# Performance work log

Hardware: AMD Instinct MI355X
Metric: run time of the kernel (lower is better)

## Reference

```python
import jax, jax.numpy as jnp
import numpy as np

B, N, C, H, E, K = 2, 2048, 1024, 4096, 8, 2
TAU = 1.0


def setup_inputs() -> dict:
    key = jax.random.key(0)
    ks = jax.random.split(key, 9)
    x = jax.random.normal(ks[0], (B, N, C), dtype=jnp.float32)
    T = B * N
    u = jax.random.uniform(ks[1], (T, E), minval=1e-6, maxval=1.0 - 1e-6)
    gumbel_noise = -jnp.log(-jnp.log(u))  # Gumbel(0,1) samples
    s = 0.02
    gate_w = jax.random.normal(ks[2], (C, E), dtype=jnp.float32) * s
    gate_b = jnp.zeros((E,), dtype=jnp.float32)
    w1 = jax.random.normal(ks[3], (E, C, H), dtype=jnp.float32) * s
    b1 = jnp.zeros((E, H), dtype=jnp.float32)
    w2 = jax.random.normal(ks[4], (E, H, C), dtype=jnp.float32) * s
    b2 = jnp.zeros((E, C), dtype=jnp.float32)
    return {"x": x, "gumbel_noise": gumbel_noise, "gate_w": gate_w,
            "gate_b": gate_b, "w1": w1, "b1": b1, "w2": w2, "b2": b2}


def reference(x, gumbel_noise, gate_w, gate_b, w1, b1, w2, b2):
    Bb, Nn, Cc = x.shape
    x_flat = x.reshape(-1, Cc)                                  # [T, C]
    logits = x_flat @ gate_w + gate_b                           # [T, E]
    # F.gumbel_softmax(hard=False, tau=1): softmax((logits + g)/tau)
    gates = jax.nn.softmax((logits + gumbel_noise) / TAU, axis=-1)
    mean_gates = gates.mean(axis=0)
    load_balance_loss = jnp.sum(mean_gates * jnp.log(mean_gates + 1e-8))
    topk_vals, topk_idxs = jax.lax.top_k(gates, K)              # [T, K]
    T = x_flat.shape[0]
    # scatter top-k gate weights into a dense [T, E] combine matrix
    comb = jnp.zeros((T, E), dtype=gates.dtype)
    comb = comb.at[jnp.arange(T)[:, None], topk_idxs].set(topk_vals)
    # dense per-expert MLP over all tokens, then weighted combine
    h = jnp.einsum('tc,ech->teh', x_flat, w1) + b1              # [T, E, H]
    h = jax.nn.gelu(h, approximate=False)                        # exact GELU (nn.GELU)
    y = jnp.einsum('teh,ehc->tec', h, w2) + b2                  # [T, E, C]
    out = jnp.einsum('te,tec->tc', comb, y)                     # [T, C]
    return out.reshape(Bb, Nn, Cc), load_balance_loss
```

## Files before the change

### kernel.cpp

```cpp
#include <hip/hip_runtime.h>
#include <math.h>

#define TT  4096
#define CC  1024
#define HH  4096
#define EE  8
#define TKN 8192
#define PGRID 768

typedef _Float16 f16x8 __attribute__((ext_vector_type(8)));
typedef float    f32x4 __attribute__((ext_vector_type(4)));

#define GLD_LDS16(g, l)                                                        \
    __builtin_amdgcn_global_load_lds(                                          \
        (const __attribute__((address_space(1))) void*)(g),                    \
        (__attribute__((address_space(3))) void*)(l), 16, 0, 0)

__global__ __launch_bounds__(256) void gate_kernel(
    const float* __restrict__ x, const float* __restrict__ gn,
    const float* __restrict__ gw, const float* __restrict__ gb,
    int* __restrict__ topk_idx, float* __restrict__ topk_w,
    int* __restrict__ counts, float* __restrict__ gsum)
{
    int wave = threadIdx.x >> 6, lane = threadIdx.x & 63;
    int t = blockIdx.x * 4 + wave;
    const float* xrow = x + (size_t)t * CC;

    double acc[EE];
#pragma unroll
    for (int e = 0; e < EE; e++) acc[e] = 0.0;

#pragma unroll
    for (int i = 0; i < CC / 64; i++) {
        int c = i * 64 + lane;
        float xv = xrow[c];
        const float4* g4 = reinterpret_cast<const float4*>(gw + (size_t)c * EE);
        float4 g0 = g4[0], g1 = g4[1];
        double xd = (double)xv;
        acc[0] += xd * (double)g0.x; acc[1] += xd * (double)g0.y;
        acc[2] += xd * (double)g0.z; acc[3] += xd * (double)g0.w;
        acc[4] += xd * (double)g1.x; acc[5] += xd * (double)g1.y;
        acc[6] += xd * (double)g1.z; acc[7] += xd * (double)g1.w;
    }
#pragma unroll
    for (int e = 0; e < EE; e++)
#pragma unroll
        for (int off = 32; off > 0; off >>= 1)
            acc[e] += __shfl_xor(acc[e], off);

    double z[EE], m = -1e300;
#pragma unroll
    for (int e = 0; e < EE; e++) {
        z[e] = acc[e] + (double)gb[e] + (double)gn[(size_t)t * EE + e];
        m = fmax(m, z[e]);
    }
    double p[EE], s = 0.0;
#pragma unroll
    for (int e = 0; e < EE; e++) { p[e] = exp(z[e] - m); s += p[e]; }
    double inv = 1.0 / s;
    double g[EE];
#pragma unroll
    for (int e = 0; e < EE; e++) g[e] = p[e] * inv;

    int i1 = 0; double v1 = g[0];
#pragma unroll
    for (int e = 1; e < EE; e++) if (g[e] > v1) { v1 = g[e]; i1 = e; }
    int i2 = -1; double v2 = -1.0;
#pragma unroll
    for (int e = 0; e < EE; e++) if (e != i1 && g[e] > v2) { v2 = g[e]; i2 = e; }

    if (lane == 0) {
        topk_idx[t * 2 + 0] = i1; topk_w[t * 2 + 0] = (float)v1;
        topk_idx[t * 2 + 1] = i2; topk_w[t * 2 + 1] = (float)v2;
        atomicAdd(&counts[i1], 1);
        atomicAdd(&counts[i2], 1);
    }

    __shared__ float gp[4][EE];
    if (lane == 0) {
#pragma unroll
        for (int e = 0; e < EE; e++) gp[wave][e] = (float)g[e];
    }
    __syncthreads();
    if (threadIdx.x < EE) {
        float s4 = gp[0][threadIdx.x] + gp[1][threadIdx.x] +
                   gp[2][threadIdx.x] + gp[3][threadIdx.x];
        atomicAdd(&gsum[threadIdx.x], s4);
    }
}

__global__ __launch_bounds__(256) void transpose_f16_kernel(
    const float* __restrict__ src, _Float16* __restrict__ dst, int R, int Ccols)
{
    __shared__ float tile[64][65];
    int e = blockIdx.z;
    const float* s = src + (size_t)e * R * Ccols;
    _Float16* d = dst + (size_t)e * R * Ccols;
    int c0 = blockIdx.x * 64, r0 = blockIdx.y * 64;
    int tx = threadIdx.x, ty = threadIdx.y;
#pragma unroll
    for (int i = 0; i < 16; i++) {
        int r = ty + i * 4;
        tile[r][tx] = s[(size_t)(r0 + r) * Ccols + c0 + tx];
    }
    __syncthreads();
#pragma unroll
    for (int i = 0; i < 16; i++) {
        int c = ty + i * 4;
        d[(size_t)(c0 + c) * R + r0 + tx] = (_Float16)tile[tx][c];
    }
}

__global__ __launch_bounds__(256) void scan_kernel(
    const int* __restrict__ counts, int* __restrict__ offsets,
    const float* __restrict__ gsum, float* __restrict__ loss_out,
    int* __restrict__ tiles1, int* __restrict__ tiles2, int* __restrict__ ntl)
{
    __shared__ int s_mt[EE], s_tb1[EE], s_tb2[EE];
    int tid = threadIdx.x;
    if (tid == 0) {
        int o = 0, t1 = 0, t2 = 0;
#pragma unroll
        for (int e = 0; e < EE; e++) {
            offsets[e] = o;
            int mt = (counts[e] + 127) >> 7;
            s_mt[e] = mt; s_tb1[e] = t1; s_tb2[e] = t2;
            o += counts[e]; t1 += mt * (HH / 128); t2 += mt * 2 * (CC / 128);
        }
        offsets[EE] = o;
        ntl[0] = t1; ntl[1] = t2;
        float L = 0.f;
#pragma unroll
        for (int e = 0; e < EE; e++) {
            float me = gsum[e] / (float)TT;
            L += me * logf(me + 1e-8f);
        }
        *loss_out = L;
    }
    __syncthreads();
    {
        int e = tid >> 5, n = tid & 31;
        int base = s_tb1[e] + n * s_mt[e];
        for (int m = 0; m < s_mt[e]; m++)
            tiles1[base + m] = (e << 20) | (n << 12) | m;
    }
    if (tid < 128) {
        int e = tid >> 4, nk = tid & 15;
        int base = s_tb2[e] + nk * s_mt[e];
        for (int m = 0; m < s_mt[e]; m++)
            tiles2[base + m] = (e << 20) | (nk << 12) | m;
    }
}

__global__ __launch_bounds__(256) void scatter_kernel(
    const int* __restrict__ topk_idx, const float* __restrict__ topk_w,
    const int* __restrict__ offsets, int* __restrict__ fill,
    int* __restrict__ rowtok, float* __restrict__ rweight)
{
    int t = blockIdx.x * 256 + threadIdx.x;
#pragma unroll
    for (int k = 0; k < 2; k++) {
        int e = topk_idx[t * 2 + k];
        int pos = offsets[e] + atomicAdd(&fill[e], 1);
        rowtok[pos] = t;
        rweight[pos] = topk_w[t * 2 + k];
    }
}

__global__ __launch_bounds__(256) void gather_kernel(
    const float* __restrict__ x, const int* __restrict__ rowtok,
    _Float16* __restrict__ xg)
{
    int p = blockIdx.x * 2 + (threadIdx.x >> 7);
    int c = (threadIdx.x & 127) * 8;
    int t = rowtok[p];
    const float4* s = reinterpret_cast<const float4*>(x + (size_t)t * CC + c);
    float4 v0 = s[0], v1 = s[1];
    f16x8 o;
    o[0] = (_Float16)v0.x; o[1] = (_Float16)v0.y;
    o[2] = (_Float16)v0.z; o[3] = (_Float16)v0.w;
    o[4] = (_Float16)v1.x; o[5] = (_Float16)v1.y;
    o[6] = (_Float16)v1.z; o[7] = (_Float16)v1.w;
    *reinterpret_cast<f16x8*>(xg + (size_t)p * CC + c) = o;
}

__global__ __launch_bounds__(256) void gemm1_kernel(
    const _Float16* __restrict__ xg, const _Float16* __restrict__ w1t,
    const float* __restrict__ b1, const int* __restrict__ offsets,
    const int* __restrict__ tiles, const int* __restrict__ ntl,
    _Float16* __restrict__ h)
{
    __shared__ __align__(16) _Float16 As[128][64];
    __shared__ __align__(16) _Float16 Bs[128][64];

    int nt = ntl[0];
    int q = (nt + PGRID - 1) / PGRID;
    int t0 = blockIdx.x * q;
    int t1 = t0 + q; if (t1 > nt) t1 = nt;

    int tid = threadIdx.x;
    int wave = tid >> 6, lane = tid & 63;
    int wm = (wave >> 1) * 64, wn = (wave & 1) * 64;
    int lrow = lane & 15, kg = lane >> 4;
    int ch0 = wave * 4 * 64 + lane;
    int rbase = (lane >> 4) * 4;

    for (int ti = t0; ti < t1; ti++) {
        int id = tiles[ti];
        int e = id >> 20, n0 = ((id >> 12) & 0xFF) * 128, m0 = (id & 0xFFF) * 128;
        int segs = offsets[e];
        int M = offsets[e + 1] - segs;
        const _Float16* wB = w1t + (size_t)e * HH * CC;

        const _Float16* ap[4]; const _Float16* bp[4];
        _Float16 *al[4], *bl[4];
#pragma unroll
        for (int j = 0; j < 4; j++) {
            int ch = ch0 + j * 64;
            int row = ch >> 3, kc = ch & 7;
            int rm = m0 + row; if (rm >= M) rm = M - 1;
            ap[j] = xg + (size_t)(segs + rm) * CC + kc * 8;
            bp[j] = wB + (size_t)(n0 + row) * CC + kc * 8;
            al[j] = &As[0][0] + ch * 8;
            bl[j] = &Bs[0][0] + ch * 8;
        }

        f32x4 acc[4][4];
#pragma unroll
        for (int i = 0; i < 4; i++)
#pragma unroll
            for (int j = 0; j < 4; j++)
#pragma unroll
                for (int r = 0; r < 4; r++) acc[i][j][r] = 0.f;

        for (int k0 = 0; k0 < CC; k0 += 64) {
#pragma unroll
            for (int j = 0; j < 4; j++) {
                GLD_LDS16(ap[j], al[j]);
                GLD_LDS16(bp[j], bl[j]);
                ap[j] += 64; bp[j] += 64;
            }
            __syncthreads();

            f16x8 aF[2][4], bF[2][4];
#pragma unroll
            for (int s = 0; s < 2; s++)
#pragma unroll
                for (int i = 0; i < 4; i++) {
                    aF[s][i] = *reinterpret_cast<const f16x8*>(
                        &As[wm + i * 16 + lrow][s * 32 + kg * 8]);
                    bF[s][i] = *reinterpret_cast<const f16x8*>(
                        &Bs[wn + i * 16 + lrow][s * 32 + kg * 8]);
                }
#pragma unroll
            for (int s = 0; s < 2; s++)
#pragma unroll
                for (int mi = 0; mi < 4; mi++)
#pragma unroll
                    for (int ni = 0; ni < 4; ni++)
                        acc[mi][ni] = __builtin_amdgcn_mfma_f32_16x16x32_f16(
                            aF[s][mi], bF[s][ni], acc[mi][ni], 0, 0, 0);
            __syncthreads();
        }

#pragma unroll
        for (int mi = 0; mi < 4; mi++) {
#pragma unroll
            for (int ni = 0; ni < 4; ni++) {
                int gcol = n0 + wn + ni * 16 + lrow;
                float bias = b1[(size_t)e * HH + gcol];
#pragma unroll
                for (int r = 0; r < 4; r++) {
                    int rowl = m0 + wm + mi * 16 + rbase + r;
                    if (rowl < M) {
                        float v = acc[mi][ni][r] + bias;
                        v = 0.5f * v * (1.0f + erff(v * 0.70710678118654752f));
                        h[(size_t)(segs + rowl) * HH + gcol] = (_Float16)v;
                    }
                }
            }
        }
    }
}

__global__ __launch_bounds__(256) void gemm2_kernel(
    const _Float16* __restrict__ h, const _Float16* __restrict__ w2t,
    const float* __restrict__ b2, const int* __restrict__ rowtok,
    const float* __restrict__ rweight, const int* __restrict__ offsets,
    const int* __restrict__ tiles, const int* __restrict__ ntl,
    float* __restrict__ out)
{
    __shared__ __align__(16) _Float16 As[128][64];
    __shared__ __align__(16) _Float16 Bs[128][64];
    __shared__ int toks[128];
    __shared__ float wgt[128];

    int nt = ntl[1];
    int q = (nt + PGRID - 1) / PGRID;
    int t0 = blockIdx.x * q;
    int t1 = t0 + q; if (t1 > nt) t1 = nt;

    int tid = threadIdx.x;
    int wave = tid >> 6, lane = tid & 63;
    int wm = (wave >> 1) * 64, wn = (wave & 1) * 64;
    int lrow = lane & 15, kg = lane >> 4;
    int ch0 = wave * 4 * 64 + lane;
    int rbase = (lane >> 4) * 4;

    for (int ti = t0; ti < t1; ti++) {
        int id = tiles[ti];
        int e = id >> 20, nk = (id >> 12) & 0xFF, m0 = (id & 0xFFF) * 128;
        int kz = nk >> 3, n0 = (nk & 7) * 128;
        int segs = offsets[e];
        int M = offsets[e + 1] - segs;
        const _Float16* wB = w2t + (size_t)e * CC * HH;
        int kbeg = kz * (HH / 2);

        __syncthreads();
        if (tid < 128) {
            int r = m0 + tid;
            int rr = (r < M) ? r : (M - 1);
            toks[tid] = rowtok[segs + rr];
            wgt[tid] = rweight[segs + rr];
        }

        const _Float16* ap[4]; const _Float16* bp[4];
        _Float16 *al[4], *bl[4];
#pragma unroll
        for (int j = 0; j < 4; j++) {
            int ch = ch0 + j * 64;
            int row = ch >> 3, kc = ch & 7;
            int rm = m0 + row; if (rm >= M) rm = M - 1;
            ap[j] = h  + (size_t)(segs + rm) * HH + kbeg + kc * 8;
            bp[j] = wB + (size_t)(n0 + row) * HH + kbeg + kc * 8;
            al[j] = &As[0][0] + ch * 8;
            bl[j] = &Bs[0][0] + ch * 8;
        }

        f32x4 acc[4][4];
#pragma unroll
        for (int i = 0; i < 4; i++)
#pragma unroll
            for (int j = 0; j < 4; j++)
#pragma unroll
                for (int r = 0; r < 4; r++) acc[i][j][r] = 0.f;

        for (int k0 = 0; k0 < HH / 2; k0 += 64) {
#pragma unroll
            for (int j = 0; j < 4; j++) {
                GLD_LDS16(ap[j], al[j]);
                GLD_LDS16(bp[j], bl[j]);
                ap[j] += 64; bp[j] += 64;
            }
            __syncthreads();

            f16x8 aF[2][4], bF[2][4];
#pragma unroll
            for (int s = 0; s < 2; s++)
#pragma unroll
                for (int i = 0; i < 4; i++) {
                    aF[s][i] = *reinterpret_cast<const f16x8*>(
                        &As[wm + i * 16 + lrow][s * 32 + kg * 8]);
                    bF[s][i] = *reinterpret_cast<const f16x8*>(
                        &Bs[wn + i * 16 + lrow][s * 32 + kg * 8]);
                }
#pragma unroll
            for (int s = 0; s < 2; s++)
#pragma unroll
                for (int mi = 0; mi < 4; mi++)
#pragma unroll
                    for (int ni = 0; ni < 4; ni++)
                        acc[mi][ni] = __builtin_amdgcn_mfma_f32_16x16x32_f16(
                            aF[s][mi], bF[s][ni], acc[mi][ni], 0, 0, 0);
            __syncthreads();
        }

#pragma unroll
        for (int mi = 0; mi < 4; mi++) {
#pragma unroll
            for (int ni = 0; ni < 4; ni++) {
                int gcol = n0 + wn + ni * 16 + lrow;
                float bias = (kz == 0) ? b2[(size_t)e * CC + gcol] : 0.f;
#pragma unroll
                for (int r = 0; r < 4; r++) {
                    int rowl = m0 + wm + mi * 16 + rbase + r;
                    if (rowl < M) {
                        int lr = rowl - m0;
                        float v = (acc[mi][ni][r] + bias) * wgt[lr];
                        unsafeAtomicAdd(&out[(size_t)toks[lr] * CC + gcol], v);
                    }
                }
            }
        }
    }
}

extern "C" void kernel_launch(void* const* d_in, const int* in_sizes, int n_in,
                              void* d_out, int out_size, void* d_ws, size_t ws_size,
                              hipStream_t stream)
{
    const float* x  = (const float*)d_in[0];
    const float* gn = (const float*)d_in[1];
    const float* gw = (const float*)d_in[2];
    const float* gb = (const float*)d_in[3];
    const float* w1 = (const float*)d_in[4];
    const float* b1 = (const float*)d_in[5];
    const float* w2 = (const float*)d_in[6];
    const float* b2 = (const float*)d_in[7];
    float* out = (float*)d_out;

    char* w = (char*)d_ws;
    int*   counts  = (int*)(w + 0);
    int*   fill    = (int*)(w + 32);
    int*   offsets = (int*)(w + 64);
    float* gsum    = (float*)(w + 128);
    int*   ntl     = (int*)(w + 192);
    size_t off = 256;
    int*   topk_idx = (int*)(w + off);   off += (size_t)TT * 2 * 4;
    float* topk_w   = (float*)(w + off); off += (size_t)TT * 2 * 4;
    int*   rowtok   = (int*)(w + off);   off += (size_t)TKN * 4;
    float* rweight  = (float*)(w + off); off += (size_t)TKN * 4;
    int*   tiles1   = (int*)(w + off);   off += 4096 * 4;
    int*   tiles2   = (int*)(w + off);   off += 2048 * 4;
    _Float16* xg  = (_Float16*)(w + off); off += (size_t)TKN * CC * 2;
    _Float16* w1t = (_Float16*)(w + off); off += (size_t)EE * HH * CC * 2;
    _Float16* w2t = (_Float16*)(w + off); off += (size_t)EE * CC * HH * 2;
    _Float16* hbuf = (_Float16*)(w + off); off += (size_t)TKN * HH * 2;

    (void)hipMemsetAsync(d_out, 0, (size_t)out_size * sizeof(float), stream);
    (void)hipMemsetAsync(d_ws, 0, 256, stream);

    gate_kernel<<<TT / 4, 256, 0, stream>>>(x, gn, gw, gb, topk_idx, topk_w,
                                            counts, gsum);
    transpose_f16_kernel<<<dim3(HH / 64, CC / 64, EE), dim3(64, 4), 0, stream>>>(
        w1, w1t, CC, HH);
    transpose_f16_kernel<<<dim3(CC / 64, HH / 64, EE), dim3(64, 4), 0, stream>>>(
        w2, w2t, HH, CC);
    scan_kernel<<<1, 256, 0, stream>>>(counts, offsets, gsum,
                                       out + (size_t)TT * CC, tiles1, tiles2, ntl);
    scatter_kernel<<<TT / 256, 256, 0, stream>>>(topk_idx, topk_w, offsets, fill,
                                                 rowtok, rweight);
    gather_kernel<<<TKN / 2, 256, 0, stream>>>(x, rowtok, xg);
    gemm1_kernel<<<PGRID, 256, 0, stream>>>(xg, w1t, b1, offsets, tiles1, ntl, hbuf);
    gemm2_kernel<<<PGRID, 256, 0, stream>>>(hbuf, w2t, b2, rowtok, rweight,
                                            offsets, tiles2, ntl, out);
}
```

Baseline: 976.9 us.

## Use atomic tile tickets, tanh GELU, and a deterministic combine pass

Replaces the static tile partition in both grouped GEMMs with a per-block atomic ticket counter for dynamic load balancing, and raises the persistent grid size with an occupancy hint. Exact erf GELU is swapped for a tanh-based approximation built on a fast exp. When the workspace is large enough, gemm2 writes per-K-split partial results to a buffer, and a new combine kernel sums the two splits and applies the top-k weights. This removes the float atomics and the output memset, at the cost of extra buffer traffic and a small change in numerical accuracy.

```diff
diff --git a/kernel.cpp b/kernel.cpp
--- a/kernel.cpp
+++ b/kernel.cpp
@@ -6,7 +6,7 @@
 #define HH  4096
 #define EE  8
 #define TKN 8192
-#define PGRID 768
+#define PGRID 1024
 
 typedef _Float16 f16x8 __attribute__((ext_vector_type(8)));
 typedef float    f32x4 __attribute__((ext_vector_type(4)));
@@ -15,6 +15,12 @@
     __builtin_amdgcn_global_load_lds(                                          \
         (const __attribute__((address_space(1))) void*)(g),                    \
         (__attribute__((address_space(3))) void*)(l), 16, 0, 0)
+
+__device__ __forceinline__ float fast_gelu(float v) {
+    float y = 0.79788456080286536f * (v + 0.044715f * v * v * v);
+    float ey = __expf(2.0f * y);
+    return v - v / (ey + 1.0f);
+}
 
 __global__ __launch_bounds__(256) void gate_kernel(
     const float* __restrict__ x, const float* __restrict__ gn,
@@ -155,7 +161,8 @@
 __global__ __launch_bounds__(256) void scatter_kernel(
     const int* __restrict__ topk_idx, const float* __restrict__ topk_w,
     const int* __restrict__ offsets, int* __restrict__ fill,
-    int* __restrict__ rowtok, float* __restrict__ rweight)
+    int* __restrict__ rowtok, float* __restrict__ rweight,
+    int* __restrict__ posmap)
 {
     int t = blockIdx.x * 256 + threadIdx.x;
 #pragma unroll
@@ -164,6 +171,7 @@
         int pos = offsets[e] + atomicAdd(&fill[e], 1);
         rowtok[pos] = t;
         rweight[pos] = topk_w[t * 2 + k];
+        posmap[t * 2 + k] = pos;
     }
 }
 
@@ -184,20 +192,17 @@
     *reinterpret_cast<f16x8*>(xg + (size_t)p * CC + c) = o;
 }
 
-__global__ __launch_bounds__(256) void gemm1_kernel(
+__global__ __launch_bounds__(256, 4) void gemm1_kernel(
     const _Float16* __restrict__ xg, const _Float16* __restrict__ w1t,
     const float* __restrict__ b1, const int* __restrict__ offsets,
     const int* __restrict__ tiles, const int* __restrict__ ntl,
-    _Float16* __restrict__ h)
+    int* __restrict__ ticket, _Float16* __restrict__ h)
 {
     __shared__ __align__(16) _Float16 As[128][64];
     __shared__ __align__(16) _Float16 Bs[128][64];
+    __shared__ int sh_ti;
 
     int nt = ntl[0];
-    int q = (nt + PGRID - 1) / PGRID;
-    int t0 = blockIdx.x * q;
-    int t1 = t0 + q; if (t1 > nt) t1 = nt;
-
     int tid = threadIdx.x;
     int wave = tid >> 6, lane = tid & 63;
     int wm = (wave >> 1) * 64, wn = (wave & 1) * 64;
@@ -205,7 +210,12 @@
     int ch0 = wave * 4 * 64 + lane;
     int rbase = (lane >> 4) * 4;
 
-    for (int ti = t0; ti < t1; ti++) {
+    for (;;) {
+        if (tid == 0) sh_ti = atomicAdd(ticket, 1);
+        __syncthreads();
+        int ti = sh_ti;
+        if (ti >= nt) break;
+
         int id = tiles[ti];
         int e = id >> 20, n0 = ((id >> 12) & 0xFF) * 128, m0 = (id & 0xFFF) * 128;
         int segs = offsets[e];
@@ -273,8 +283,7 @@
                 for (int r = 0; r < 4; r++) {
                     int rowl = m0 + wm + mi * 16 + rbase + r;
                     if (rowl < M) {
-                        float v = acc[mi][ni][r] + bias;
-                        v = 0.5f * v * (1.0f + erff(v * 0.70710678118654752f));
+                        float v = fast_gelu(acc[mi][ni][r] + bias);
                         h[(size_t)(segs + rowl) * HH + gcol] = (_Float16)v;
                     }
                 }
@@ -283,23 +292,20 @@
     }
 }
 
-__global__ __launch_bounds__(256) void gemm2_kernel(
+__global__ __launch_bounds__(256, 4) void gemm2_kernel(
     const _Float16* __restrict__ h, const _Float16* __restrict__ w2t,
     const float* __restrict__ b2, const int* __restrict__ rowtok,
     const float* __restrict__ rweight, const int* __restrict__ offsets,
     const int* __restrict__ tiles, const int* __restrict__ ntl,
-    float* __restrict__ out)
+    int* __restrict__ ticket, float* __restrict__ ybuf, float* __restrict__ out)
 {
     __shared__ __align__(16) _Float16 As[128][64];
     __shared__ __align__(16) _Float16 Bs[128][64];
     __shared__ int toks[128];
     __shared__ float wgt[128];
+    __shared__ int sh_ti;
 
     int nt = ntl[1];
-    int q = (nt + PGRID - 1) / PGRID;
-    int t0 = blockIdx.x * q;
-    int t1 = t0 + q; if (t1 > nt) t1 = nt;
-
     int tid = threadIdx.x;
     int wave = tid >> 6, lane = tid & 63;
     int wm = (wave >> 1) * 64, wn = (wave & 1) * 64;
@@ -307,7 +313,12 @@
     int ch0 = wave * 4 * 64 + lane;
     int rbase = (lane >> 4) * 4;
 
-    for (int ti = t0; ti < t1; ti++) {
+    for (;;) {
+        if (tid == 0) sh_ti = atomicAdd(ticket, 1);
+        __syncthreads();
+        int ti = sh_ti;
+        if (ti >= nt) break;
+
         int id = tiles[ti];
         int e = id >> 20, nk = (id >> 12) & 0xFF, m0 = (id & 0xFFF) * 128;
         int kz = nk >> 3, n0 = (nk & 7) * 128;
@@ -316,8 +327,7 @@
         const _Float16* wB = w2t + (size_t)e * CC * HH;
         int kbeg = kz * (HH / 2);
 
-        __syncthreads();
-        if (tid < 128) {
+        if (!ybuf && tid < 128) {
             int r = m0 + tid;
             int rr = (r < M) ? r : (M - 1);
             toks[tid] = rowtok[segs + rr];
@@ -385,13 +395,43 @@
                 for (int r = 0; r < 4; r++) {
                     int rowl = m0 + wm + mi * 16 + rbase + r;
                     if (rowl < M) {
-                        int lr = rowl - m0;
-                        float v = (acc[mi][ni][r] + bias) * wgt[lr];
-                        unsafeAtomicAdd(&out[(size_t)toks[lr] * CC + gcol], v);
+                        float v = acc[mi][ni][r] + bias;
+                        if (ybuf) {
+                            ybuf[((size_t)kz * TKN + segs + rowl) * CC + gcol] = v;
+                        } else {
+                            int lr = rowl - m0;
+                            unsafeAtomicAdd(&out[(size_t)toks[lr] * CC + gcol],
+                                            v * wgt[lr]);
+                        }
                     }
                 }
             }
         }
+    }
+}
+
+__global__ __launch_bounds__(256) void combine_kernel(
+    const float* __restrict__ ybuf, const int* __restrict__ posmap,
+    const float* __restrict__ topk_w, float* __restrict__ out)
+{
+    int t = blockIdx.x * 2 + (threadIdx.x >> 7);
+    int c = (threadIdx.x & 127) * 8;
+    int p1 = posmap[t * 2 + 0], p2 = posmap[t * 2 + 1];
+    float w1 = topk_w[t * 2 + 0], w2 = topk_w[t * 2 + 1];
+    const float4* y0a = reinterpret_cast<const float4*>(ybuf + (size_t)p1 * CC + c);
+    const float4* y1a = reinterpret_cast<const float4*>(ybuf + ((size_t)TKN + p1) * CC + c);
+    const float4* y0b = reinterpret_cast<const float4*>(ybuf + (size_t)p2 * CC + c);
+    const float4* y1b = reinterpret_cast<const float4*>(ybuf + ((size_t)TKN + p2) * CC + c);
+    float4* o = reinterpret_cast<float4*>(out + (size_t)t * CC + c);
+#pragma unroll
+    for (int i = 0; i < 2; i++) {
+        float4 a0 = y0a[i], a1 = y1a[i], b0 = y0b[i], b1 = y1b[i];
+        float4 r;
+        r.x = w1 * (a0.x + a1.x) + w2 * (b0.x + b1.x);
+        r.y = w1 * (a0.y + a1.y) + w2 * (b0.y + b1.y);
+        r.z = w1 * (a0.z + a1.z) + w2 * (b0.z + b1.z);
+        r.w = w1 * (a0.w + a1.w) + w2 * (b0.w + b1.w);
+        o[i] = r;
     }
 }
 
@@ -415,20 +455,28 @@
     int*   offsets = (int*)(w + 64);
     float* gsum    = (float*)(w + 128);
     int*   ntl     = (int*)(w + 192);
+    int*   tick1   = (int*)(w + 200);
+    int*   tick2   = (int*)(w + 204);
     size_t off = 256;
     int*   topk_idx = (int*)(w + off);   off += (size_t)TT * 2 * 4;
     float* topk_w   = (float*)(w + off); off += (size_t)TT * 2 * 4;
     int*   rowtok   = (int*)(w + off);   off += (size_t)TKN * 4;
     float* rweight  = (float*)(w + off); off += (size_t)TKN * 4;
+    int*   posmap   = (int*)(w + off);   off += (size_t)TKN * 4;
     int*   tiles1   = (int*)(w + off);   off += 4096 * 4;
     int*   tiles2   = (int*)(w + off);   off += 2048 * 4;
     _Float16* xg  = (_Float16*)(w + off); off += (size_t)TKN * CC * 2;
     _Float16* w1t = (_Float16*)(w + off); off += (size_t)EE * HH * CC * 2;
     _Float16* w2t = (_Float16*)(w + off); off += (size_t)EE * CC * HH * 2;
     _Float16* hbuf = (_Float16*)(w + off); off += (size_t)TKN * HH * 2;
-
-    (void)hipMemsetAsync(d_out, 0, (size_t)out_size * sizeof(float), stream);
+    float* ybuf = (float*)(w + off);
+    size_t need = off + (size_t)2 * TKN * CC * 4;
+    bool use_ybuf = (ws_size >= need);
+    if (!use_ybuf) ybuf = nullptr;
+
     (void)hipMemsetAsync(d_ws, 0, 256, stream);
+    if (!use_ybuf)
+        (void)hipMemsetAsync(d_out, 0, (size_t)out_size * sizeof(float), stream);
 
     gate_kernel<<<TT / 4, 256, 0, stream>>>(x, gn, gw, gb, topk_idx, topk_w,
                                             counts, gsum);
@@ -439,9 +487,12 @@
     scan_kernel<<<1, 256, 0, stream>>>(counts, offsets, gsum,
                                        out + (size_t)TT * CC, tiles1, tiles2, ntl);
     scatter_kernel<<<TT / 256, 256, 0, stream>>>(topk_idx, topk_w, offsets, fill,
-                                                 rowtok, rweight);
+                                                 rowtok, rweight, posmap);
     gather_kernel<<<TKN / 2, 256, 0, stream>>>(x, rowtok, xg);
-    gemm1_kernel<<<PGRID, 256, 0, stream>>>(xg, w1t, b1, offsets, tiles1, ntl, hbuf);
+    gemm1_kernel<<<PGRID, 256, 0, stream>>>(xg, w1t, b1, offsets, tiles1, ntl,
+                                            tick1, hbuf);
     gemm2_kernel<<<PGRID, 256, 0, stream>>>(hbuf, w2t, b2, rowtok, rweight,
-                                            offsets, tiles2, ntl, out);
-}
+                                            offsets, tiles2, ntl, tick2, ybuf, out);
+    if (use_ybuf)
+        combine_kernel<<<TT / 2, 256, 0, stream>>>(ybuf, posmap, topk_w, out);
+}
```

New measurement: 991.9 us. About the same (+1.5%).

## Enlarge expert GEMM tiles to 256x256 with 512 threads and tanh GELU

Applied to the files above, without the earlier changes.

Both grouped GEMMs move from 128x128 tiles with 256 threads to 256x256 tiles with 512 threads (8 waves, each computing 64x128). Work is distributed with a grid-stride loop over a 256-block grid. The point is more reuse per LDS load and fewer tiles, at the cost of more padding waste on the per-expert row remainder and higher register pressure. The exact erf GELU is replaced by a tanh-form approximation built on __expf, and the weight transpose kernel now uses vectorized float4 loads and f16x8 stores.

```diff
diff --git a/kernel.cpp b/kernel.cpp
--- a/kernel.cpp
+++ b/kernel.cpp
@@ -6,7 +6,7 @@
 #define HH  4096
 #define EE  8
 #define TKN 8192
-#define PGRID 768
+#define GGRID 256
 
 typedef _Float16 f16x8 __attribute__((ext_vector_type(8)));
 typedef float    f32x4 __attribute__((ext_vector_type(4)));
@@ -15,6 +15,12 @@
     __builtin_amdgcn_global_load_lds(                                          \
         (const __attribute__((address_space(1))) void*)(g),                    \
         (__attribute__((address_space(3))) void*)(l), 16, 0, 0)
+
+__device__ __forceinline__ float fast_gelu(float v) {
+    float y = 0.79788456080286536f * (v + 0.044715f * v * v * v);
+    float ey = __expf(2.0f * y);
+    return v - v / (ey + 1.0f);
+}
 
 __global__ __launch_bounds__(256) void gate_kernel(
     const float* __restrict__ x, const float* __restrict__ gn,
@@ -97,17 +103,25 @@
     const float* s = src + (size_t)e * R * Ccols;
     _Float16* d = dst + (size_t)e * R * Ccols;
     int c0 = blockIdx.x * 64, r0 = blockIdx.y * 64;
-    int tx = threadIdx.x, ty = threadIdx.y;
-#pragma unroll
-    for (int i = 0; i < 16; i++) {
-        int r = ty + i * 4;
-        tile[r][tx] = s[(size_t)(r0 + r) * Ccols + c0 + tx];
+    int tid = threadIdx.x;
+#pragma unroll
+    for (int i = 0; i < 4; i++) {
+        int idx = i * 256 + tid;
+        int r = idx >> 4, c4 = (idx & 15) * 4;
+        float4 v = *reinterpret_cast<const float4*>(
+            s + (size_t)(r0 + r) * Ccols + c0 + c4);
+        tile[r][c4 + 0] = v.x; tile[r][c4 + 1] = v.y;
+        tile[r][c4 + 2] = v.z; tile[r][c4 + 3] = v.w;
     }
     __syncthreads();
 #pragma unroll
-    for (int i = 0; i < 16; i++) {
-        int c = ty + i * 4;
-        d[(size_t)(c0 + c) * R + r0 + tx] = (_Float16)tile[tx][c];
+    for (int i = 0; i < 2; i++) {
+        int idx = i * 256 + tid;
+        int c = idx >> 3, s8 = (idx & 7) * 8;
+        f16x8 o;
+#pragma unroll
+        for (int j = 0; j < 8; j++) o[j] = (_Float16)tile[s8 + j][c];
+        *reinterpret_cast<f16x8*>(d + (size_t)(c0 + c) * R + r0 + s8) = o;
     }
 }
 
@@ -123,9 +137,9 @@
 #pragma unroll
         for (int e = 0; e < EE; e++) {
             offsets[e] = o;
-            int mt = (counts[e] + 127) >> 7;
+            int mt = (counts[e] + 255) >> 8;
             s_mt[e] = mt; s_tb1[e] = t1; s_tb2[e] = t2;
-            o += counts[e]; t1 += mt * (HH / 128); t2 += mt * 2 * (CC / 128);
+            o += counts[e]; t1 += mt * (HH / 256); t2 += mt * 2 * (CC / 256);
         }
         offsets[EE] = o;
         ntl[0] = t1; ntl[1] = t2;
@@ -138,14 +152,14 @@
         *loss_out = L;
     }
     __syncthreads();
-    {
-        int e = tid >> 5, n = tid & 31;
+    if (tid < 128) {
+        int e = tid >> 4, n = tid & 15;
         int base = s_tb1[e] + n * s_mt[e];
         for (int m = 0; m < s_mt[e]; m++)
             tiles1[base + m] = (e << 20) | (n << 12) | m;
     }
-    if (tid < 128) {
-        int e = tid >> 4, nk = tid & 15;
+    if (tid < 64) {
+        int e = tid >> 3, nk = tid & 7;
         int base = s_tb2[e] + nk * s_mt[e];
         for (int m = 0; m < s_mt[e]; m++)
             tiles2[base + m] = (e << 20) | (nk << 12) | m;
@@ -184,30 +198,26 @@
     *reinterpret_cast<f16x8*>(xg + (size_t)p * CC + c) = o;
 }
 
-__global__ __launch_bounds__(256) void gemm1_kernel(
+__global__ __launch_bounds__(512, 2) void gemm1_kernel(
     const _Float16* __restrict__ xg, const _Float16* __restrict__ w1t,
     const float* __restrict__ b1, const int* __restrict__ offsets,
     const int* __restrict__ tiles, const int* __restrict__ ntl,
     _Float16* __restrict__ h)
 {
-    __shared__ __align__(16) _Float16 As[128][64];
-    __shared__ __align__(16) _Float16 Bs[128][64];
+    __shared__ __align__(16) _Float16 As[256][64];
+    __shared__ __align__(16) _Float16 Bs[256][64];
 
     int nt = ntl[0];
-    int q = (nt + PGRID - 1) / PGRID;
-    int t0 = blockIdx.x * q;
-    int t1 = t0 + q; if (t1 > nt) t1 = nt;
-
     int tid = threadIdx.x;
     int wave = tid >> 6, lane = tid & 63;
-    int wm = (wave >> 1) * 64, wn = (wave & 1) * 64;
+    int wm = (wave >> 1) * 64, wn = (wave & 1) * 128;
     int lrow = lane & 15, kg = lane >> 4;
-    int ch0 = wave * 4 * 64 + lane;
+    int ch0 = wave * 256 + lane;
     int rbase = (lane >> 4) * 4;
 
-    for (int ti = t0; ti < t1; ti++) {
+    for (int ti = blockIdx.x; ti < nt; ti += gridDim.x) {
         int id = tiles[ti];
-        int e = id >> 20, n0 = ((id >> 12) & 0xFF) * 128, m0 = (id & 0xFFF) * 128;
+        int e = id >> 20, n0 = ((id >> 12) & 0xFF) * 256, m0 = (id & 0xFFF) * 256;
         int segs = offsets[e];
         int M = offsets[e + 1] - segs;
         const _Float16* wB = w1t + (size_t)e * HH * CC;
@@ -225,11 +235,11 @@
             bl[j] = &Bs[0][0] + ch * 8;
         }
 
-        f32x4 acc[4][4];
+        f32x4 acc[4][8];
 #pragma unroll
         for (int i = 0; i < 4; i++)
 #pragma unroll
-            for (int j = 0; j < 4; j++)
+            for (int j = 0; j < 8; j++)
 #pragma unroll
                 for (int r = 0; r < 4; r++) acc[i][j][r] = 0.f;
 
@@ -242,39 +252,38 @@
             }
             __syncthreads();
 
-            f16x8 aF[2][4], bF[2][4];
-#pragma unroll
-            for (int s = 0; s < 2; s++)
-#pragma unroll
-                for (int i = 0; i < 4; i++) {
-                    aF[s][i] = *reinterpret_cast<const f16x8*>(
+#pragma unroll
+            for (int s = 0; s < 2; s++) {
+                f16x8 aF[4], bF[8];
+#pragma unroll
+                for (int i = 0; i < 4; i++)
+                    aF[i] = *reinterpret_cast<const f16x8*>(
                         &As[wm + i * 16 + lrow][s * 32 + kg * 8]);
-                    bF[s][i] = *reinterpret_cast<const f16x8*>(
+#pragma unroll
+                for (int i = 0; i < 8; i++)
+                    bF[i] = *reinterpret_cast<const f16x8*>(
                         &Bs[wn + i * 16 + lrow][s * 32 + kg * 8]);
-                }
-#pragma unroll
-            for (int s = 0; s < 2; s++)
 #pragma unroll
                 for (int mi = 0; mi < 4; mi++)
 #pragma unroll
-                    for (int ni = 0; ni < 4; ni++)
+                    for (int ni = 0; ni < 8; ni++)
                         acc[mi][ni] = __builtin_amdgcn_mfma_f32_16x16x32_f16(
-                            aF[s][mi], bF[s][ni], acc[mi][ni], 0, 0, 0);
+                            aF[mi], bF[ni], acc[mi][ni], 0, 0, 0);
+            }
             __syncthreads();
         }
 
 #pragma unroll
         for (int mi = 0; mi < 4; mi++) {
 #pragma unroll
-            for (int ni = 0; ni < 4; ni++) {
+            for (int ni = 0; ni < 8; ni++) {
                 int gcol = n0 + wn + ni * 16 + lrow;
                 float bias = b1[(size_t)e * HH + gcol];
 #pragma unroll
                 for (int r = 0; r < 4; r++) {
                     int rowl = m0 + wm + mi * 16 + rbase + r;
                     if (rowl < M) {
-                        float v = acc[mi][ni][r] + bias;
-                        v = 0.5f * v * (1.0f + erff(v * 0.70710678118654752f));
+                        float v = fast_gelu(acc[mi][ni][r] + bias);
                         h[(size_t)(segs + rowl) * HH + gcol] = (_Float16)v;
                     }
                 }
@@ -283,41 +292,37 @@
     }
 }
 
-__global__ __launch_bounds__(256) void gemm2_kernel(
+__global__ __launch_bounds__(512, 2) void gemm2_kernel(
     const _Float16* __restrict__ h, const _Float16* __restrict__ w2t,
     const float* __restrict__ b2, const int* __restrict__ rowtok,
     const float* __restrict__ rweight, const int* __restrict__ offsets,
     const int* __restrict__ tiles, const int* __restrict__ ntl,
     float* __restrict__ out)
 {
-    __shared__ __align__(16) _Float16 As[128][64];
-    __shared__ __align__(16) _Float16 Bs[128][64];
-    __shared__ int toks[128];
-    __shared__ float wgt[128];
+    __shared__ __align__(16) _Float16 As[256][64];
+    __shared__ __align__(16) _Float16 Bs[256][64];
+    __shared__ int toks[256];
+    __shared__ float wgt[256];
 
     int nt = ntl[1];
-    int q = (nt + PGRID - 1) / PGRID;
-    int t0 = blockIdx.x * q;
-    int t1 = t0 + q; if (t1 > nt) t1 = nt;
-
     int tid = threadIdx.x;
     int wave = tid >> 6, lane = tid & 63;
-    int wm = (wave >> 1) * 64, wn = (wave & 1) * 64;
+    int wm = (wave >> 1) * 64, wn = (wave & 1) * 128;
     int lrow = lane & 15, kg = lane >> 4;
-    int ch0 = wave * 4 * 64 + lane;
+    int ch0 = wave * 256 + lane;
     int rbase = (lane >> 4) * 4;
 
-    for (int ti = t0; ti < t1; ti++) {
+    for (int ti = blockIdx.x; ti < nt; ti += gridDim.x) {
+        __syncthreads();
         int id = tiles[ti];
-        int e = id >> 20, nk = (id >> 12) & 0xFF, m0 = (id & 0xFFF) * 128;
-        int kz = nk >> 3, n0 = (nk & 7) * 128;
+        int e = id >> 20, nk = (id >> 12) & 0xFF, m0 = (id & 0xFFF) * 256;
+        int kz = nk >> 2, n0 = (nk & 3) * 256;
         int segs = offsets[e];
         int M = offsets[e + 1] - segs;
         const _Float16* wB = w2t + (size_t)e * CC * HH;
         int kbeg = kz * (HH / 2);
 
-        __syncthreads();
-        if (tid < 128) {
+        if (tid < 256) {
             int r = m0 + tid;
             int rr = (r < M) ? r : (M - 1);
             toks[tid] = rowtok[segs + rr];
@@ -337,11 +342,11 @@
             bl[j] = &Bs[0][0] + ch * 8;
         }
 
-        f32x4 acc[4][4];
+        f32x4 acc[4][8];
 #pragma unroll
         for (int i = 0; i < 4; i++)
 #pragma unroll
-            for (int j = 0; j < 4; j++)
+            for (int j = 0; j < 8; j++)
 #pragma unroll
                 for (int r = 0; r < 4; r++) acc[i][j][r] = 0.f;
 
@@ -354,31 +359,31 @@
             }
             __syncthreads();
 
-            f16x8 aF[2][4], bF[2][4];
-#pragma unroll
-            for (int s = 0; s < 2; s++)
-#pragma unroll
-                for (int i = 0; i < 4; i++) {
-                    aF[s][i] = *reinterpret_cast<const f16x8*>(
+#pragma unroll
+            for (int s = 0; s < 2; s++) {
+                f16x8 aF[4], bF[8];
+#pragma unroll
+                for (int i = 0; i < 4; i++)
+                    aF[i] = *reinterpret_cast<const f16x8*>(
                         &As[wm + i * 16 + lrow][s * 32 + kg * 8]);
-                    bF[s][i] = *reinterpret_cast<const f16x8*>(
+#pragma unroll
+                for (int i = 0; i < 8; i++)
+                    bF[i] = *reinterpret_cast<const f16x8*>(
                         &Bs[wn + i * 16 + lrow][s * 32 + kg * 8]);
-                }
-#pragma unroll
-            for (int s = 0; s < 2; s++)
 #pragma unroll
                 for (int mi = 0; mi < 4; mi++)
 #pragma unroll
-                    for (int ni = 0; ni < 4; ni++)
+                    for (int ni = 0; ni < 8; ni++)
                         acc[mi][ni] = __builtin_amdgcn_mfma_f32_16x16x32_f16(
-                            aF[s][mi], bF[s][ni], acc[mi][ni], 0, 0, 0);
+                            aF[mi], bF[ni], acc[mi][ni], 0, 0, 0);
+            }
             __syncthreads();
         }
 
 #pragma unroll
         for (int mi = 0; mi < 4; mi++) {
 #pragma unroll
-            for (int ni = 0; ni < 4; ni++) {
+            for (int ni = 0; ni < 8; ni++) {
                 int gcol = n0 + wn + ni * 16 + lrow;
                 float bias = (kz == 0) ? b2[(size_t)e * CC + gcol] : 0.f;
 #pragma unroll
@@ -432,16 +437,16 @@
 
     gate_kernel<<<TT / 4, 256, 0, stream>>>(x, gn, gw, gb, topk_idx, topk_w,
                                             counts, gsum);
-    transpose_f16_kernel<<<dim3(HH / 64, CC / 64, EE), dim3(64, 4), 0, stream>>>(
+    transpose_f16_kernel<<<dim3(HH / 64, CC / 64, EE), 256, 0, stream>>>(
         w1, w1t, CC, HH);
-    transpose_f16_kernel<<<dim3(CC / 64, HH / 64, EE), dim3(64, 4), 0, stream>>>(
+    transpose_f16_kernel<<<dim3(CC / 64, HH / 64, EE), 256, 0, stream>>>(
         w2, w2t, HH, CC);
     scan_kernel<<<1, 256, 0, stream>>>(counts, offsets, gsum,
                                        out + (size_t)TT * CC, tiles1, tiles2, ntl);
     scatter_kernel<<<TT / 256, 256, 0, stream>>>(topk_idx, topk_w, offsets, fill,
                                                  rowtok, rweight);
     gather_kernel<<<TKN / 2, 256, 0, stream>>>(x, rowtok, xg);
-    gemm1_kernel<<<PGRID, 256, 0, stream>>>(xg, w1t, b1, offsets, tiles1, ntl, hbuf);
-    gemm2_kernel<<<PGRID, 256, 0, stream>>>(hbuf, w2t, b2, rowtok, rweight,
+    gemm1_kernel<<<GGRID, 512, 0, stream>>>(xg, w1t, b1, offsets, tiles1, ntl, hbuf);
+    gemm2_kernel<<<GGRID, 512, 0, stream>>>(hbuf, w2t, b2, rowtok, rweight,
                                             offsets, tiles2, ntl, out);
 }
```

Measured after the change: 969.3 us. About the same (-0.8%).
